# Kernel tuning notes

Measured on AMD Instinct MI355X. Metric: run time of the kernel, lower is better.

The kernel has to match this reference:

```python
import jax, jax.numpy as jnp
import numpy as np

B, C, E = 4, 2048, 1024
H, D = 16, 64  # num_heads, head_size

def setup_inputs() -> dict:
    key = jax.random.key(0)
    kx, kk, kq, kv, ko = jax.random.split(key, 5)
    s = 1.0 / np.sqrt(E)
    so = 1.0 / np.sqrt(H * D)
    return {
        "x": jax.random.normal(kx, (B, C, E), dtype=jnp.float32),
        "Wk": jax.random.uniform(kk, (H * D, E), jnp.float32, -s, s),
        "Wq": jax.random.uniform(kq, (H * D, E), jnp.float32, -s, s),
        "Wv": jax.random.uniform(kv, (H * D, E), jnp.float32, -s, s),
        "Wo": jax.random.uniform(ko, (E, H * D), jnp.float32, -so, so),
    }

def reference(x, Wk, Wq, Wv, Wo):
    b, c, e = x.shape
    # projections -> [B, H, C, D]
    def proj(W):
        return (x @ W.T).reshape(b, c, H, D).transpose(0, 2, 1, 3)
    k = proj(Wk)
    q = proj(Wq)
    v = proj(Wv)
    # scores [B, H, C, C]; mask applied before scaling (as in source; -inf*scale = -inf)
    sa = jnp.einsum("bhqd,bhkd->bhqk", q, k)
    mask = ~jnp.tril(jnp.ones((c, c), dtype=bool))  # True above diagonal
    masked = jnp.where(mask, -jnp.inf, sa)
    scale = 1.0 / np.sqrt(D)
    attn = jax.nn.softmax(masked * scale, axis=-1)
    out = jnp.einsum("bhqk,bhkd->bhqd", attn, v)  # [B, H, C, D]
    flat = out.transpose(0, 2, 1, 3).reshape(b, c, H * D)
    return flat @ Wo.T
```

## Files before the change

### kernel.cpp

```cpp
#include <hip/hip_runtime.h>
#include <hip/hip_bf16.h>

typedef __bf16 bf16x8 __attribute__((ext_vector_type(8)));
typedef __bf16 bf16x4 __attribute__((ext_vector_type(4)));
typedef float f32x4 __attribute__((ext_vector_type(4)));

#define NEG_INF (-__builtin_inff())

__global__ void cvt_all(const float* __restrict__ x,
                        const float* __restrict__ Wq, const float* __restrict__ Wk,
                        const float* __restrict__ Wv, const float* __restrict__ Wo,
                        __bf16* __restrict__ xb, __bf16* __restrict__ wqkv,
                        __bf16* __restrict__ wo_b) {
    int i = (blockIdx.x * blockDim.x + threadIdx.x) * 4;
    const float* src;
    __bf16* dst;
    int off;
    if (i < 8388608) {
        src = x; dst = xb; off = i;
    } else {
        int j = i - 8388608;
        int sel = j >> 20;
        off = j & 1048575;
        src = (sel == 0) ? Wq : (sel == 1) ? Wk : (sel == 2) ? Wv : Wo;
        dst = (sel < 3) ? (wqkv + (size_t)sel * 1048576) : wo_b;
    }
    float4 v = *(const float4*)(src + off);
    bf16x4 o;
    o[0] = (__bf16)v.x; o[1] = (__bf16)v.y; o[2] = (__bf16)v.z; o[3] = (__bf16)v.w;
    *(bf16x4*)(dst + off) = o;
}

template <int MODE>
__launch_bounds__(256, 3)
__global__ void gemm_bt(const __bf16* __restrict__ A, const __bf16* __restrict__ Bm,
                        void* __restrict__ Out, int M, int N, int K) {
    __shared__ __align__(1024) char smem[32768];
    const int tid = threadIdx.x;
    const int w = tid >> 6, lane = tid & 63;
    const int lr = lane & 15, lg = lane >> 4;
    const int wm0 = (w >> 1) * 64, wn0 = (w & 1) * 64;

    const int nbx = gridDim.x;
    int id = blockIdx.y * nbx + blockIdx.x;
    int q8 = (nbx * gridDim.y) >> 3;
    int vid = (id & 7) * q8 + (id >> 3);
    const int m0 = (vid / nbx) * 128, n0 = (vid % nbx) * 128;

    const char* Ab = (const char*)A;
    const char* Bb = (const char*)Bm;

    f32x4 acc[4][4] = {};

    const int s_row8 = lane >> 3;
    const int s_col16 = lane & 7;

    const int nt = K >> 6;
    for (int t = 0; t < nt; ++t) {
#pragma unroll
        for (int r = 0; r < 4; ++r) {
            int c = w * 4 + r;
            int row = c * 8 + s_row8;
            const char* srcA = Ab + ((size_t)(m0 + row) * K + t * 64) * 2 + s_col16 * 16;
            const char* srcB = Bb + ((size_t)(n0 + row) * K + t * 64) * 2 + s_col16 * 16;
            __builtin_amdgcn_global_load_lds(
                (const __attribute__((address_space(1))) void*)srcA,
                (__attribute__((address_space(3))) void*)(smem + c * 1024), 16, 0, 0);
            __builtin_amdgcn_global_load_lds(
                (const __attribute__((address_space(1))) void*)srcB,
                (__attribute__((address_space(3))) void*)(smem + 16384 + c * 1024), 16, 0, 0);
        }
        __syncthreads();

#pragma unroll
        for (int kk = 0; kk < 2; ++kk) {
            bf16x8 af[4], bf[4];
#pragma unroll
            for (int mi = 0; mi < 4; ++mi)
                af[mi] = *(const bf16x8*)(smem + (wm0 + mi * 16 + lr) * 128 + kk * 64 + lg * 16);
#pragma unroll
            for (int ni = 0; ni < 4; ++ni)
                bf[ni] = *(const bf16x8*)(smem + 16384 + (wn0 + ni * 16 + lr) * 128 + kk * 64 + lg * 16);
            __builtin_amdgcn_s_setprio(1);
#pragma unroll
            for (int mi = 0; mi < 4; ++mi)
#pragma unroll
                for (int ni = 0; ni < 4; ++ni)
                    acc[mi][ni] = __builtin_amdgcn_mfma_f32_16x16x32_bf16(
                        af[mi], bf[ni], acc[mi][ni], 0, 0, 0);
            __builtin_amdgcn_s_setprio(0);
        }
        __syncthreads();
    }

#pragma unroll
    for (int mi = 0; mi < 4; ++mi)
#pragma unroll
        for (int ni = 0; ni < 4; ++ni)
#pragma unroll
            for (int r = 0; r < 4; ++r) {
                int m = m0 + wm0 + mi * 16 + lg * 4 + r;
                int n = n0 + wn0 + ni * 16 + lr;
                float v = acc[mi][ni][r];
                if (MODE == 0) {
                    int proj = n >> 10, nn = n & 1023;
                    int h = nn >> 6, d = nn & 63;
                    int bb = m >> 11, c = m & 2047;
                    if (proj == 2) {
                        ((__bf16*)Out)[(size_t)2 * 8388608 +
                                       ((size_t)((bb * 16 + h) * 64 + d)) * 2048 + c] = (__bf16)v;
                    } else {
                        float scale = (proj == 0) ? 0.125f : 1.0f;
                        ((__bf16*)Out)[(size_t)proj * 8388608 +
                                       ((size_t)(bb * 16 + h) * 2048 + c) * 64 + d] =
                            (__bf16)(v * scale);
                    }
                } else {
                    ((float*)Out)[(size_t)m * N + n] = v;
                }
            }
}

__device__ __forceinline__ unsigned swz(unsigned d) {
    return d ^ (((d >> 7) & 7) << 4);
}

__launch_bounds__(256, 4)
__global__ void attn_fwd(const __bf16* __restrict__ Q, const __bf16* __restrict__ K,
                         const __bf16* __restrict__ Vt, __bf16* __restrict__ Aout) {
    __shared__ char smem[40960];
    const int id = blockIdx.x;
    const int vid = (id & 7) * 128 + (id >> 3);
    const int bh = vid >> 4, pr = vid & 15;
    const int w = threadIdx.x >> 6, lane = threadIdx.x & 63;
    const int lr = lane & 15, lg = lane >> 4;
    const char* Kb  = (const char*)(K  + (size_t)bh * 2048 * 64);
    const char* Vtb = (const char*)(Vt + (size_t)bh * 64 * 2048);
    const __bf16* Qb = Q + (size_t)bh * 2048 * 64;
    const int b = bh >> 4, h = bh & 15;
    char* Pb = smem + 32768 + w * 2048;

    const int qta = 31 - pr, qtb = pr;
    const int q0a = qta * 64 + w * 16, q0b = qtb * 64 + w * 16;

    bf16x8 qfa[2], qfb[2];
#pragma unroll
    for (int kk = 0; kk < 2; ++kk) {
        qfa[kk] = *(const bf16x8*)&Qb[(size_t)(q0a + lr) * 64 + kk * 32 + lg * 8];
        qfb[kk] = *(const bf16x8*)&Qb[(size_t)(q0b + lr) * 64 + kk * 32 + lg * 8];
    }

    f32x4 oa[4] = {}, ob[4] = {};
    float ma = NEG_INF, la = 0.f, mb = NEG_INF, lb = 0.f;

    {
        char* kd = smem;
        char* vd = smem + 16384;
#pragma unroll
        for (int i = 0; i < 2; ++i) {
            unsigned c = (unsigned)(w * 2 + i);
            unsigned d = c * 1024 + (unsigned)lane * 16;
            unsigned bs = swz(d);
            __builtin_amdgcn_global_load_lds(
                (const __attribute__((address_space(1))) void*)(Kb + bs),
                (__attribute__((address_space(3))) void*)(kd + c * 1024), 16, 0, 0);
            unsigned row = bs >> 7, colb = bs & 127;
            __builtin_amdgcn_global_load_lds(
                (const __attribute__((address_space(1))) void*)(Vtb + (size_t)row * 4096 + colb),
                (__attribute__((address_space(3))) void*)(vd + c * 1024), 16, 0, 0);
        }
    }

    const int nt = qta + 1;
    for (int t = 0; t < nt; ++t) {
        __syncthreads();
        if (t + 1 < nt) {
            char* kd = smem + ((t + 1) & 1) * 8192;
            char* vd = smem + 16384 + ((t + 1) & 1) * 8192;
#pragma unroll
            for (int i = 0; i < 2; ++i) {
                unsigned c = (unsigned)(w * 2 + i);
                unsigned d = c * 1024 + (unsigned)lane * 16;
                unsigned bs = swz(d);
                __builtin_amdgcn_global_load_lds(
                    (const __attribute__((address_space(1))) void*)(Kb + (size_t)(t + 1) * 8192 + bs),
                    (__attribute__((address_space(3))) void*)(kd + c * 1024), 16, 0, 0);
                unsigned row = bs >> 7, colb = bs & 127;
                __builtin_amdgcn_global_load_lds(
                    (const __attribute__((address_space(1))) void*)(Vtb + (size_t)row * 4096 +
                                                                   (size_t)(t + 1) * 128 + colb),
                    (__attribute__((address_space(3))) void*)(vd + c * 1024), 16, 0, 0);
            }
        }
        const char* Ks = smem + (t & 1) * 8192;
        const char* Vs = smem + 16384 + (t & 1) * 8192;
        const int k0 = t * 64;

        auto process = [&](const bf16x8 (&qf)[2], int q0, bool diag,
                           f32x4 (&o)[4], float& m, float& l) {
            f32x4 s[4] = {};
#pragma unroll
            for (int kk = 0; kk < 2; ++kk)
#pragma unroll
                for (int sub = 0; sub < 4; ++sub) {
                    bf16x8 kf = *(const bf16x8*)(Ks + swz((unsigned)((sub * 16 + lr) * 128 + kk * 64 + lg * 16)));
                    s[sub] = __builtin_amdgcn_mfma_f32_16x16x32_bf16(kf, qf[kk], s[sub], 0, 0, 0);
                }
            if (diag) {
#pragma unroll
                for (int sub = 0; sub < 4; ++sub)
#pragma unroll
                    for (int r = 0; r < 4; ++r)
                        if (k0 + sub * 16 + lg * 4 + r > q0 + lr) s[sub][r] = NEG_INF;
            }
            float mloc = NEG_INF;
#pragma unroll
            for (int sub = 0; sub < 4; ++sub)
#pragma unroll
                for (int r = 0; r < 4; ++r) mloc = fmaxf(mloc, s[sub][r]);
            mloc = fmaxf(mloc, __shfl_xor(mloc, 16));
            mloc = fmaxf(mloc, __shfl_xor(mloc, 32));
            float mnew = fmaxf(m, mloc);
            float alpha = __expf(m - mnew);
            float rs = 0.f;
#pragma unroll
            for (int sub = 0; sub < 4; ++sub)
#pragma unroll
                for (int r = 0; r < 4; ++r) {
                    float p = __expf(s[sub][r] - mnew);
                    s[sub][r] = p;
                    rs += p;
                }
            rs += __shfl_xor(rs, 16);
            rs += __shfl_xor(rs, 32);
            l = l * alpha + rs;
            m = mnew;
#pragma unroll
            for (int ni = 0; ni < 4; ++ni) o[ni] *= alpha;

#pragma unroll
            for (int sub = 0; sub < 4; ++sub) {
                bf16x4 pk;
#pragma unroll
                for (int r = 0; r < 4; ++r) pk[r] = (__bf16)s[sub][r];
                *(bf16x4*)(Pb + swz((unsigned)(lr * 128 + sub * 32 + lg * 8))) = pk;
            }
            bf16x8 pfr[2];
#pragma unroll
            for (int kk = 0; kk < 2; ++kk)
                pfr[kk] = *(const bf16x8*)(Pb + swz((unsigned)(lr * 128 + kk * 64 + lg * 16)));

#pragma unroll
            for (int kk = 0; kk < 2; ++kk)
#pragma unroll
                for (int ni = 0; ni < 4; ++ni) {
                    bf16x8 vf = *(const bf16x8*)(Vs + swz((unsigned)((ni * 16 + lr) * 128 + kk * 64 + lg * 16)));
                    o[ni] = __builtin_amdgcn_mfma_f32_16x16x32_bf16(vf, pfr[kk], o[ni], 0, 0, 0);
                }
        };

        process(qfa, q0a, t == qta, oa, ma, la);
        if (t <= qtb) process(qfb, q0b, t == qtb, ob, mb, lb);
    }

    float ra = 1.0f / la, rb = 1.0f / lb;
#pragma unroll
    for (int ni = 0; ni < 4; ++ni) {
        bf16x4 va, vb;
#pragma unroll
        for (int r = 0; r < 4; ++r) {
            va[r] = (__bf16)(oa[ni][r] * ra);
            vb[r] = (__bf16)(ob[ni][r] * rb);
        }
        *(bf16x4*)&Aout[((size_t)b * 2048 + q0a + lr) * 1024 + h * 64 + ni * 16 + lg * 4] = va;
        *(bf16x4*)&Aout[((size_t)b * 2048 + q0b + lr) * 1024 + h * 64 + ni * 16 + lg * 4] = vb;
    }
}

extern "C" void kernel_launch(void* const* d_in, const int* in_sizes, int n_in,
                              void* d_out, int out_size, void* d_ws, size_t ws_size,
                              hipStream_t stream) {
    const float* x  = (const float*)d_in[0];
    const float* Wk = (const float*)d_in[1];
    const float* Wq = (const float*)d_in[2];
    const float* Wv = (const float*)d_in[3];
    const float* Wo = (const float*)d_in[4];

    char* ws = (char*)d_ws;
    __bf16* xb   = (__bf16*)(ws);
    __bf16* wqkv = (__bf16*)(ws + 16777216);
    __bf16* wo_b = (__bf16*)(ws + 23068672);
    __bf16* qkv  = (__bf16*)(ws + 25165824);
    __bf16* aout = (__bf16*)(ws + 75497472);
    float* out = (float*)d_out;

    cvt_all<<<12288, 256, 0, stream>>>(x, Wq, Wk, Wv, Wo, xb, wqkv, wo_b);

    gemm_bt<0><<<dim3(24, 64), 256, 0, stream>>>(xb, wqkv, qkv, 8192, 3072, 1024);
    attn_fwd<<<dim3(1024), 256, 0, stream>>>(qkv, qkv + 8388608, qkv + 16777216, aout);
    gemm_bt<1><<<dim3(8, 64), 256, 0, stream>>>(aout, wo_b, out, 8192, 1024, 1024);
}
```

Measured before the change: 187.5 us.

## Read K/V fragments directly from global memory instead of LDS double-buffering

Removes the LDS staging of K and V tiles (global_load_lds double buffer plus per-tile __syncthreads) and has each wave load its K and V^T MFMA fragments straight from global memory, shrinking shared memory to the P scratch only. It also folds log2(e) into the Q scale so softmax can use exp2f, and wraps MFMA groups in s_setprio. The goal is to drop barrier and LDS traffic and raise occupancy, but every wave now reloads the same K/V data from global or L2 with no cross-wave sharing and no explicit prefetch, so load latency may be exposed.

```diff
diff --git a/kernel.cpp b/kernel.cpp
--- a/kernel.cpp
+++ b/kernel.cpp
@@ -110,7 +110,7 @@
                         ((__bf16*)Out)[(size_t)2 * 8388608 +
                                        ((size_t)((bb * 16 + h) * 64 + d)) * 2048 + c] = (__bf16)v;
                     } else {
-                        float scale = (proj == 0) ? 0.125f : 1.0f;
+                        float scale = (proj == 0) ? 0.18033688089f : 1.0f;
                         ((__bf16*)Out)[(size_t)proj * 8388608 +
                                        ((size_t)(bb * 16 + h) * 2048 + c) * 64 + d] =
                             (__bf16)(v * scale);
@@ -128,7 +128,7 @@
 __launch_bounds__(256, 4)
 __global__ void attn_fwd(const __bf16* __restrict__ Q, const __bf16* __restrict__ K,
                          const __bf16* __restrict__ Vt, __bf16* __restrict__ Aout) {
-    __shared__ char smem[40960];
+    __shared__ char smem[8192];
     const int id = blockIdx.x;
     const int vid = (id & 7) * 128 + (id >> 3);
     const int bh = vid >> 4, pr = vid & 15;
@@ -138,7 +138,7 @@
     const char* Vtb = (const char*)(Vt + (size_t)bh * 64 * 2048);
     const __bf16* Qb = Q + (size_t)bh * 2048 * 64;
     const int b = bh >> 4, h = bh & 15;
-    char* Pb = smem + 32768 + w * 2048;
+    char* Pb = smem + w * 2048;
 
     const int qta = 31 - pr, qtb = pr;
     const int q0a = qta * 64 + w * 16, q0b = qtb * 64 + w * 16;
@@ -153,59 +153,27 @@
     f32x4 oa[4] = {}, ob[4] = {};
     float ma = NEG_INF, la = 0.f, mb = NEG_INF, lb = 0.f;
 
-    {
-        char* kd = smem;
-        char* vd = smem + 16384;
-#pragma unroll
-        for (int i = 0; i < 2; ++i) {
-            unsigned c = (unsigned)(w * 2 + i);
-            unsigned d = c * 1024 + (unsigned)lane * 16;
-            unsigned bs = swz(d);
-            __builtin_amdgcn_global_load_lds(
-                (const __attribute__((address_space(1))) void*)(Kb + bs),
-                (__attribute__((address_space(3))) void*)(kd + c * 1024), 16, 0, 0);
-            unsigned row = bs >> 7, colb = bs & 127;
-            __builtin_amdgcn_global_load_lds(
-                (const __attribute__((address_space(1))) void*)(Vtb + (size_t)row * 4096 + colb),
-                (__attribute__((address_space(3))) void*)(vd + c * 1024), 16, 0, 0);
-        }
-    }
-
     const int nt = qta + 1;
     for (int t = 0; t < nt; ++t) {
-        __syncthreads();
-        if (t + 1 < nt) {
-            char* kd = smem + ((t + 1) & 1) * 8192;
-            char* vd = smem + 16384 + ((t + 1) & 1) * 8192;
-#pragma unroll
-            for (int i = 0; i < 2; ++i) {
-                unsigned c = (unsigned)(w * 2 + i);
-                unsigned d = c * 1024 + (unsigned)lane * 16;
-                unsigned bs = swz(d);
-                __builtin_amdgcn_global_load_lds(
-                    (const __attribute__((address_space(1))) void*)(Kb + (size_t)(t + 1) * 8192 + bs),
-                    (__attribute__((address_space(3))) void*)(kd + c * 1024), 16, 0, 0);
-                unsigned row = bs >> 7, colb = bs & 127;
-                __builtin_amdgcn_global_load_lds(
-                    (const __attribute__((address_space(1))) void*)(Vtb + (size_t)row * 4096 +
-                                                                   (size_t)(t + 1) * 128 + colb),
-                    (__attribute__((address_space(3))) void*)(vd + c * 1024), 16, 0, 0);
-            }
-        }
-        const char* Ks = smem + (t & 1) * 8192;
-        const char* Vs = smem + 16384 + (t & 1) * 8192;
+        const char* Kt  = Kb + (size_t)t * 8192;
+        const char* Vte = Vtb + (size_t)t * 128;
         const int k0 = t * 64;
 
         auto process = [&](const bf16x8 (&qf)[2], int q0, bool diag,
                            f32x4 (&o)[4], float& m, float& l) {
             f32x4 s[4] = {};
 #pragma unroll
-            for (int kk = 0; kk < 2; ++kk)
-#pragma unroll
-                for (int sub = 0; sub < 4; ++sub) {
-                    bf16x8 kf = *(const bf16x8*)(Ks + swz((unsigned)((sub * 16 + lr) * 128 + kk * 64 + lg * 16)));
-                    s[sub] = __builtin_amdgcn_mfma_f32_16x16x32_bf16(kf, qf[kk], s[sub], 0, 0, 0);
-                }
+            for (int kk = 0; kk < 2; ++kk) {
+                bf16x8 kf[4];
+#pragma unroll
+                for (int sub = 0; sub < 4; ++sub)
+                    kf[sub] = *(const bf16x8*)(Kt + (size_t)(sub * 16 + lr) * 128 + kk * 64 + lg * 16);
+                __builtin_amdgcn_s_setprio(1);
+#pragma unroll
+                for (int sub = 0; sub < 4; ++sub)
+                    s[sub] = __builtin_amdgcn_mfma_f32_16x16x32_bf16(kf[sub], qf[kk], s[sub], 0, 0, 0);
+                __builtin_amdgcn_s_setprio(0);
+            }
             if (diag) {
 #pragma unroll
                 for (int sub = 0; sub < 4; ++sub)
@@ -221,13 +189,13 @@
             mloc = fmaxf(mloc, __shfl_xor(mloc, 16));
             mloc = fmaxf(mloc, __shfl_xor(mloc, 32));
             float mnew = fmaxf(m, mloc);
-            float alpha = __expf(m - mnew);
+            float alpha = exp2f(m - mnew);
             float rs = 0.f;
 #pragma unroll
             for (int sub = 0; sub < 4; ++sub)
 #pragma unroll
                 for (int r = 0; r < 4; ++r) {
-                    float p = __expf(s[sub][r] - mnew);
+                    float p = exp2f(s[sub][r] - mnew);
                     s[sub][r] = p;
                     rs += p;
                 }
@@ -251,12 +219,17 @@
                 pfr[kk] = *(const bf16x8*)(Pb + swz((unsigned)(lr * 128 + kk * 64 + lg * 16)));
 
 #pragma unroll
-            for (int kk = 0; kk < 2; ++kk)
-#pragma unroll
-                for (int ni = 0; ni < 4; ++ni) {
-                    bf16x8 vf = *(const bf16x8*)(Vs + swz((unsigned)((ni * 16 + lr) * 128 + kk * 64 + lg * 16)));
-                    o[ni] = __builtin_amdgcn_mfma_f32_16x16x32_bf16(vf, pfr[kk], o[ni], 0, 0, 0);
-                }
+            for (int kk = 0; kk < 2; ++kk) {
+                bf16x8 vf[4];
+#pragma unroll
+                for (int ni = 0; ni < 4; ++ni)
+                    vf[ni] = *(const bf16x8*)(Vte + (size_t)(ni * 16 + lr) * 4096 + kk * 64 + lg * 16);
+                __builtin_amdgcn_s_setprio(1);
+#pragma unroll
+                for (int ni = 0; ni < 4; ++ni)
+                    o[ni] = __builtin_amdgcn_mfma_f32_16x16x32_bf16(vf[ni], pfr[kk], o[ni], 0, 0, 0);
+                __builtin_amdgcn_s_setprio(0);
+            }
         };
 
         process(qfa, q0a, t == qta, oa, ma, la);
```

Result: slower. 361.3 us (+92.7%).
